# Optimization experiments

Hardware: AMD Instinct MI355X
Metric: run time of the kernel (lower is better)

Reference implementation:

```python
import jax, jax.numpy as jnp
import numpy as np

N = 100000
E = 1600000
IN, HID, OUT = 64, 128, 64
EPS = 1e-5


def _sage_conv(x, src, dst, w_l, b_l, w_r):
    # PyG SAGEConv (mean aggr): out = lin_l(mean_{j in N(i)} x_j) + lin_r(x_i)
    msgs = x[src]                                   # [E, d] gather
    agg = jax.ops.segment_sum(msgs, dst, num_segments=N)  # [N, d]
    deg = jax.ops.segment_sum(jnp.ones((E,), x.dtype), dst, num_segments=N)
    agg = agg / jnp.maximum(deg, 1.0)[:, None]      # mean over neighbors
    return agg @ w_l.T + b_l + x @ w_r.T


def _bn_eval(x, gamma, beta, mean, var):
    return (x - mean) * jax.lax.rsqrt(var + EPS) * gamma + beta


def setup_inputs() -> dict:
    key = jax.random.key(0)
    ks = jax.random.split(key, 16)
    x = jax.random.normal(ks[0], (N, IN), jnp.float32)
    edge_index = jax.random.randint(ks[1], (2, E), 0, N, jnp.int32)
    s1 = 1.0 / np.sqrt(IN)
    s2 = 1.0 / np.sqrt(HID)
    return {
        "x": x,
        "edge_index": edge_index,
        "w1l": jax.random.uniform(ks[2], (HID, IN), jnp.float32, -s1, s1),
        "b1l": jax.random.uniform(ks[3], (HID,), jnp.float32, -s1, s1),
        "w1r": jax.random.uniform(ks[4], (HID, IN), jnp.float32, -s1, s1),
        "bn1_gamma": jax.random.uniform(ks[5], (HID,), jnp.float32, 0.5, 1.5),
        "bn1_beta": jax.random.normal(ks[6], (HID,), jnp.float32) * 0.1,
        "bn1_mean": jax.random.normal(ks[7], (HID,), jnp.float32) * 0.1,
        "bn1_var": jax.random.uniform(ks[8], (HID,), jnp.float32, 0.5, 1.5),
        "w2l": jax.random.uniform(ks[9], (OUT, HID), jnp.float32, -s2, s2),
        "b2l": jax.random.uniform(ks[10], (OUT,), jnp.float32, -s2, s2),
        "w2r": jax.random.uniform(ks[11], (OUT, HID), jnp.float32, -s2, s2),
        "bn2_gamma": jax.random.uniform(ks[12], (OUT,), jnp.float32, 0.5, 1.5),
        "bn2_beta": jax.random.normal(ks[13], (OUT,), jnp.float32) * 0.1,
        "bn2_mean": jax.random.normal(ks[14], (OUT,), jnp.float32) * 0.1,
        "bn2_var": jax.random.uniform(ks[15], (OUT,), jnp.float32, 0.5, 1.5),
    }


def reference(x, edge_index, w1l, b1l, w1r, bn1_gamma, bn1_beta, bn1_mean, bn1_var,
              w2l, b2l, w2r, bn2_gamma, bn2_beta, bn2_mean, bn2_var):
    src, dst = edge_index[0], edge_index[1]
    # layer 1: SAGEConv -> BN -> ReLU (dropout is identity in eval mode)
    h = _sage_conv(x, src, dst, w1l, b1l, w1r)
    h = jax.nn.relu(_bn_eval(h, bn1_gamma, bn1_beta, bn1_mean, bn1_var))
    # layer 2: SAGEConv -> BN
    h = _sage_conv(h, src, dst, w2l, b2l, w2r)
    return _bn_eval(h, bn2_gamma, bn2_beta, bn2_mean, bn2_var)
```

## Files before the change

### kernel.cpp

```cpp
#include <hip/hip_runtime.h>

#define NN 100000
#define NE 1600000
#define EPSV 1e-5f

#define NBUK 196
#define TILE 2048
#define NTIL 782
#define NPREP 6250
#define CAP  9216

typedef __attribute__((ext_vector_type(8))) short bf16x8;
typedef __attribute__((ext_vector_type(4))) float f32x4;

__device__ inline unsigned short f2bf(float f) {
  unsigned u = __builtin_bit_cast(unsigned, f);
  unsigned r = u + 0x7FFFu + ((u >> 16) & 1u);
  return (unsigned short)(r >> 16);
}
__device__ inline float bf2f(unsigned short s) {
  unsigned u = ((unsigned)s) << 16;
  return __builtin_bit_cast(float, u);
}

__device__ __forceinline__ void gload_lds16(const unsigned short* g, unsigned short* l) {
  __builtin_amdgcn_global_load_lds(
      (const __attribute__((address_space(1))) void*)g,
      (__attribute__((address_space(3))) void*)l, 16, 0, 0);
}

__global__ __launch_bounds__(256) void k_binprep(const int* __restrict__ src,
                                                 const int* __restrict__ dst,
                                                 unsigned* __restrict__ pairs,
                                                 int* __restrict__ tileCnt,
                                                 int* __restrict__ tileLo,
                                                 const float* __restrict__ x,
                                                 unsigned short* __restrict__ xb,
                                                 const float* __restrict__ w1l,
                                                 const float* __restrict__ w1r,
                                                 const float* __restrict__ w2l,
                                                 const float* __restrict__ w2r,
                                                 const float* __restrict__ b1l,
                                                 const float* __restrict__ g1,
                                                 const float* __restrict__ be1,
                                                 const float* __restrict__ m1,
                                                 const float* __restrict__ v1,
                                                 const float* __restrict__ b2l,
                                                 const float* __restrict__ g2,
                                                 const float* __restrict__ be2,
                                                 const float* __restrict__ m2,
                                                 const float* __restrict__ v2,
                                                 unsigned short* __restrict__ w1c,
                                                 unsigned short* __restrict__ w2c,
                                                 float* __restrict__ bn) {
  const int tid = threadIdx.x;
  if (blockIdx.x >= NTIL) {
    const int pb = blockIdx.x - NTIL;
    const int gi = pb * 256 + tid;
    float4 v = *(const float4*)(x + (size_t)gi * 4);
    ushort4 o;
    o.x = f2bf(v.x); o.y = f2bf(v.y); o.z = f2bf(v.z); o.w = f2bf(v.w);
    *(ushort4*)(xb + (size_t)gi * 4) = o;
    if (pb < 64) {
      int i = pb * 256 + tid;
      int oo = i >> 7, k = i & 127;
      float vv1 = (k < 64) ? w1l[oo * 64 + k] : w1r[oo * 64 + (k - 64)];
      w1c[i] = f2bf(vv1);
      float vv2 = (oo < 64) ? w2l[oo * 128 + k] : w2r[(oo - 64) * 128 + k];
      w2c[i] = f2bf(vv2);
      if (i < 128) {
        float sc = g1[i] * rsqrtf(v1[i] + EPSV);
        bn[i] = sc;
        bn[128 + i] = (b1l[i] - m1[i]) * sc + be1[i];
      }
      if (i < 64) {
        float sc = g2[i] * rsqrtf(v2[i] + EPSV);
        bn[256 + i] = sc;
        bn[320 + i] = (b2l[i] - m2[i]) * sc + be2[i];
      }
    }
    return;
  }
  __shared__ int cnt[NBUK];
  __shared__ int lo[NBUK];
  __shared__ int ts[256];
  __shared__ unsigned stage[TILE];
  const int t = blockIdx.x;
  const int e0 = t * TILE;
  const int m = min(TILE, NE - e0);

  int dreg[8], sreg[8];
#pragma unroll
  for (int u = 0; u < 8; ++u) {
    int i = u * 256 + tid;
    if (i < m) {
      dreg[u] = dst[e0 + i];
      sreg[u] = src[e0 + i];
    } else {
      dreg[u] = -1;
    }
  }

  for (int i = tid; i < NBUK; i += 256) cnt[i] = 0;
  __syncthreads();
#pragma unroll
  for (int u = 0; u < 8; ++u) {
    if (dreg[u] >= 0) atomicAdd(&cnt[dreg[u] >> 9], 1);
  }
  __syncthreads();
  int c = (tid < NBUK) ? cnt[tid] : 0;
  ts[tid] = c;
  __syncthreads();
  for (int d = 1; d < 256; d <<= 1) {
    int v = (tid >= d) ? ts[tid - d] : 0;
    __syncthreads();
    ts[tid] += v;
    __syncthreads();
  }
  if (tid < NBUK) {
    int ex = ts[tid] - c;
    lo[tid] = ex;
    cnt[tid] = ex;
  }
  __syncthreads();
#pragma unroll
  for (int u = 0; u < 8; ++u) {
    if (dreg[u] >= 0) {
      int pos = atomicAdd(&cnt[dreg[u] >> 9], 1);
      stage[pos] = ((unsigned)(dreg[u] & 511) << 17) | (unsigned)sreg[u];
    }
  }
  __syncthreads();
  for (int i = tid; i < m; i += 256) pairs[(size_t)t * TILE + i] = stage[i];
  if (tid < NBUK) {
    tileCnt[t * NBUK + tid] = cnt[tid] - lo[tid];
    tileLo[t * NBUK + tid] = lo[tid];
  }
}

__global__ __launch_bounds__(256) void k_colscan(const int* __restrict__ tileCnt,
                                                 int* __restrict__ colBase) {
  __shared__ int ts[256];
  const int tid = threadIdx.x;
  const int b = blockIdx.x;
  int v[4];
  int s = 0;
#pragma unroll
  for (int j = 0; j < 4; ++j) {
    int tt = tid * 4 + j;
    v[j] = (tt < NTIL) ? tileCnt[tt * NBUK + b] : 0;
    s += v[j];
  }
  ts[tid] = s;
  __syncthreads();
  for (int d = 1; d < 256; d <<= 1) {
    int x = (tid >= d) ? ts[tid - d] : 0;
    __syncthreads();
    ts[tid] += x;
    __syncthreads();
  }
  int run = ts[tid] - s;
#pragma unroll
  for (int j = 0; j < 4; ++j) {
    int tt = tid * 4 + j;
    if (tt < NTIL) colBase[(size_t)b * NTIL + tt] = run;
    run += v[j];
  }
}

__global__ __launch_bounds__(512) void k_build(const unsigned* __restrict__ pairs,
                                               const int* __restrict__ tileCnt,
                                               const int* __restrict__ tileLo,
                                               const int* __restrict__ colBase,
                                               int* __restrict__ deg,
                                               int* __restrict__ offset,
                                               int* __restrict__ csr) {
  __shared__ unsigned stageA[CAP];
  __shared__ unsigned stageB[CAP];
  __shared__ int colB[NTIL];
  __shared__ int tLo[NTIL];
  __shared__ int hist[512];
  __shared__ int ts[512];
  __shared__ int obase_sh, count_sh;
  const int tid = threadIdx.x;
  const int b = blockIdx.x;
  const int nbase = b * 512;
  const int nloc = min(512, NN - nbase);

  int tb = 0;
  if (tid < NBUK) {
    int cb = colBase[(size_t)tid * NTIL + (NTIL - 1)];
    int tc = tileCnt[(NTIL - 1) * NBUK + tid];
    tb = min(cb + tc, CAP);
  }
  ts[tid] = tb;
  __syncthreads();
  for (int d = 1; d < 512; d <<= 1) {
    int v = (tid >= d) ? ts[tid - d] : 0;
    __syncthreads();
    ts[tid] += v;
    __syncthreads();
  }
  if (tid == b) { obase_sh = ts[tid] - tb; count_sh = tb; }
  for (int i = tid; i < NTIL; i += 512) {
    colB[i] = colBase[(size_t)b * NTIL + i];
    tLo[i] = tileLo[i * NBUK + b];
  }
  hist[tid] = 0;
  __syncthreads();
  const int obase = obase_sh;
  const int count = count_sh;

  for (int i = tid; i < count; i += 512) {
    int a = 0, z = NTIL - 1;
    while (a < z) {
      int mid = (a + z + 1) >> 1;
      if (colB[mid] <= i) a = mid; else z = mid - 1;
    }
    stageA[i] = pairs[(size_t)a * TILE + tLo[a] + (i - colB[a])];
  }
  __syncthreads();
  for (int i = tid; i < count; i += 512) {
    atomicAdd(&hist[stageA[i] >> 17], 1);
  }
  __syncthreads();
  int s = hist[tid];
  ts[tid] = s;
  __syncthreads();
  for (int d = 1; d < 512; d <<= 1) {
    int v = (tid >= d) ? ts[tid - d] : 0;
    __syncthreads();
    ts[tid] += v;
    __syncthreads();
  }
  int ex = ts[tid] - s;
  if (tid < nloc) {
    deg[nbase + tid] = s;
    offset[nbase + tid] = obase + ex;
  }
  hist[tid] = ex;
  __syncthreads();
  for (int i = tid; i < count; i += 512) {
    unsigned e = stageA[i];
    int pos = atomicAdd(&hist[e >> 17], 1);
    stageB[pos] = e & 0x1FFFFu;
  }
  __syncthreads();
  for (int i = tid; i < count; i += 512) csr[obase + i] = (int)stageB[i];
}

__global__ __launch_bounds__(256) void k_aggregate(const unsigned short* __restrict__ xb,
                                                   const int* __restrict__ deg,
                                                   const int* __restrict__ offset,
                                                   const int* __restrict__ csr,
                                                   unsigned short* __restrict__ aggB) {
  int tid = threadIdx.x;
  int node = blockIdx.x * 32 + (tid >> 3);
  int j = tid & 7;
  int cnt = deg[node];
  const int* arow = csr + offset[node];
  float a0=0.f,a1=0.f,a2=0.f,a3=0.f,a4=0.f,a5=0.f,a6=0.f,a7=0.f;
  int k = 0;
  for (; k + 8 <= cnt; k += 8) {
    int s[8];
#pragma unroll
    for (int u = 0; u < 8; ++u) s[u] = arow[k + u];
    uint4 v[8];
#pragma unroll
    for (int u = 0; u < 8; ++u) v[u] = *(const uint4*)(xb + (size_t)s[u] * 64 + j * 8);
#pragma unroll
    for (int u = 0; u < 8; ++u) {
      a0 += bf2f(v[u].x & 0xffff); a1 += bf2f(v[u].x >> 16);
      a2 += bf2f(v[u].y & 0xffff); a3 += bf2f(v[u].y >> 16);
      a4 += bf2f(v[u].z & 0xffff); a5 += bf2f(v[u].z >> 16);
      a6 += bf2f(v[u].w & 0xffff); a7 += bf2f(v[u].w >> 16);
    }
  }
  if (k + 4 <= cnt) {
    int s[4];
#pragma unroll
    for (int u = 0; u < 4; ++u) s[u] = arow[k + u];
    uint4 v[4];
#pragma unroll
    for (int u = 0; u < 4; ++u) v[u] = *(const uint4*)(xb + (size_t)s[u] * 64 + j * 8);
#pragma unroll
    for (int u = 0; u < 4; ++u) {
      a0 += bf2f(v[u].x & 0xffff); a1 += bf2f(v[u].x >> 16);
      a2 += bf2f(v[u].y & 0xffff); a3 += bf2f(v[u].y >> 16);
      a4 += bf2f(v[u].z & 0xffff); a5 += bf2f(v[u].z >> 16);
      a6 += bf2f(v[u].w & 0xffff); a7 += bf2f(v[u].w >> 16);
    }
    k += 4;
  }
  for (; k < cnt; ++k) {
    int s = arow[k];
    uint4 v = *(const uint4*)(xb + (size_t)s * 64 + j * 8);
    a0 += bf2f(v.x & 0xffff); a1 += bf2f(v.x >> 16);
    a2 += bf2f(v.y & 0xffff); a3 += bf2f(v.y >> 16);
    a4 += bf2f(v.z & 0xffff); a5 += bf2f(v.z >> 16);
    a6 += bf2f(v.w & 0xffff); a7 += bf2f(v.w >> 16);
  }
  float inv = 1.0f / fmaxf((float)cnt, 1.0f);
  ushort4 r0, r1;
  r0.x = f2bf(a0 * inv); r0.y = f2bf(a1 * inv); r0.z = f2bf(a2 * inv); r0.w = f2bf(a3 * inv);
  r1.x = f2bf(a4 * inv); r1.y = f2bf(a5 * inv); r1.z = f2bf(a6 * inv); r1.w = f2bf(a7 * inv);
  *(ushort4*)(aggB + (size_t)node * 64 + j * 8) = r0;
  *(ushort4*)(aggB + (size_t)node * 64 + j * 8 + 4) = r1;
}

__global__ __launch_bounds__(512, 1) void k_gemm12(const unsigned short* __restrict__ aggB,
                                                   const unsigned short* __restrict__ xb,
                                                   const unsigned short* __restrict__ w1c,
                                                   const unsigned short* __restrict__ w2c,
                                                   const float* __restrict__ bn,
                                                   unsigned short* __restrict__ t,
                                                   unsigned short* __restrict__ r2) {
  __shared__ unsigned short w1lds[32 * 512];
  __shared__ unsigned short w2lds[32 * 512];
  __shared__ unsigned short hlds[8][2][16 * 128];
  __shared__ float bnlds[384];
  const int tid = threadIdx.x;
  const int w = tid >> 6;
  const int lane = tid & 63;
  const int lr = lane & 15;
  const int q = lane >> 4;
  const int tile = blockIdx.x * 8 + w;
  const int base = tile * 32;
  const int nA = base + lr, nB = base + 16 + lr;
  const int cA = min(nA, NN - 1), cB = min(nB, NN - 1);
  const int swz = (lr & 7) << 4;

#pragma unroll
  for (int it = 0; it < 4; ++it) {
    int idx = it * 512 + tid;
    int f = idx >> 6, l = idx & 63;
    int gofs = ((f >> 2) * 16 + (l & 15)) * 128 + (f & 3) * 32 + (l >> 4) * 8;
    gload_lds16(w1c + gofs, &w1lds[(it * 512 + w * 64) * 8]);
    gload_lds16(w2c + gofs, &w2lds[(it * 512 + w * 64) * 8]);
  }
  if (tid < 384) bnlds[tid] = bn[tid];

  bf16x8 fA[4], fB[4];
  {
    const unsigned short* a = aggB + (size_t)cA * 64 + q * 8;
    const unsigned short* xx = xb + (size_t)cA * 64 + q * 8;
    fA[0] = *(const bf16x8*)a;        fA[1] = *(const bf16x8*)(a + 32);
    fA[2] = *(const bf16x8*)xx;       fA[3] = *(const bf16x8*)(xx + 32);
  }
  {
    const unsigned short* a = aggB + (size_t)cB * 64 + q * 8;
    const unsigned short* xx = xb + (size_t)cB * 64 + q * 8;
    fB[0] = *(const bf16x8*)a;        fB[1] = *(const bf16x8*)(a + 32);
    fB[2] = *(const bf16x8*)xx;       fB[3] = *(const bf16x8*)(xx + 32);
  }
  __syncthreads();
  if (base >= NN) return;

  char* ldsA = (char*)&hlds[w][0][0];
  char* ldsB = (char*)&hlds[w][1][0];

#pragma unroll
  for (int ot = 0; ot < 8; ++ot) {
    const unsigned short* wp = &w1lds[(ot * 4) * 512 + lane * 8];
    bf16x8 w0 = *(const bf16x8*)(wp);
    bf16x8 w1 = *(const bf16x8*)(wp + 512);
    bf16x8 w2 = *(const bf16x8*)(wp + 1024);
    bf16x8 w3 = *(const bf16x8*)(wp + 1536);
    f32x4 aA = {0.f, 0.f, 0.f, 0.f}, aB = {0.f, 0.f, 0.f, 0.f};
    aA = __builtin_amdgcn_mfma_f32_16x16x32_bf16(w0, fA[0], aA, 0, 0, 0);
    aA = __builtin_amdgcn_mfma_f32_16x16x32_bf16(w1, fA[1], aA, 0, 0, 0);
    aA = __builtin_amdgcn_mfma_f32_16x16x32_bf16(w2, fA[2], aA, 0, 0, 0);
    aA = __builtin_amdgcn_mfma_f32_16x16x32_bf16(w3, fA[3], aA, 0, 0, 0);
    aB = __builtin_amdgcn_mfma_f32_16x16x32_bf16(w0, fB[0], aB, 0, 0, 0);
    aB = __builtin_amdgcn_mfma_f32_16x16x32_bf16(w1, fB[1], aB, 0, 0, 0);
    aB = __builtin_amdgcn_mfma_f32_16x16x32_bf16(w2, fB[2], aB, 0, 0, 0);
    aB = __builtin_amdgcn_mfma_f32_16x16x32_bf16(w3, fB[3], aB, 0, 0, 0);
    const int o = ot * 16 + q * 4;
    float4 sc = *(const float4*)&bnlds[o];
    float4 sh = *(const float4*)&bnlds[128 + o];
    ushort4 hA, hB;
    hA.x = f2bf(fmaxf(aA[0] * sc.x + sh.x, 0.f));
    hA.y = f2bf(fmaxf(aA[1] * sc.y + sh.y, 0.f));
    hA.z = f2bf(fmaxf(aA[2] * sc.z + sh.z, 0.f));
    hA.w = f2bf(fmaxf(aA[3] * sc.w + sh.w, 0.f));
    hB.x = f2bf(fmaxf(aB[0] * sc.x + sh.x, 0.f));
    hB.y = f2bf(fmaxf(aB[1] * sc.y + sh.y, 0.f));
    hB.z = f2bf(fmaxf(aB[2] * sc.z + sh.z, 0.f));
    hB.w = f2bf(fmaxf(aB[3] * sc.w + sh.w, 0.f));
    const int wb = lr * 256 + ot * 32 + q * 8;
    *(ushort4*)(ldsA + (wb ^ swz)) = hA;
    *(ushort4*)(ldsB + (wb ^ swz)) = hB;
  }

  bf16x8 hA[4], hB[4];
#pragma unroll
  for (int jj = 0; jj < 4; ++jj) {
    const int rb = lr * 256 + jj * 64 + q * 16;
    hA[jj] = *(const bf16x8*)(ldsA + (rb ^ swz));
    hB[jj] = *(const bf16x8*)(ldsB + (rb ^ swz));
  }

#pragma unroll
  for (int ot = 0; ot < 8; ++ot) {
    const unsigned short* wp = &w2lds[(ot * 4) * 512 + lane * 8];
    bf16x8 w0 = *(const bf16x8*)(wp);
    bf16x8 w1 = *(const bf16x8*)(wp + 512);
    bf16x8 w2 = *(const bf16x8*)(wp + 1024);
    bf16x8 w3 = *(const bf16x8*)(wp + 1536);
    f32x4 aA = {0.f, 0.f, 0.f, 0.f}, aB = {0.f, 0.f, 0.f, 0.f};
    aA = __builtin_amdgcn_mfma_f32_16x16x32_bf16(w0, hA[0], aA, 0, 0, 0);
    aA = __builtin_amdgcn_mfma_f32_16x16x32_bf16(w1, hA[1], aA, 0, 0, 0);
    aA = __builtin_amdgcn_mfma_f32_16x16x32_bf16(w2, hA[2], aA, 0, 0, 0);
    aA = __builtin_amdgcn_mfma_f32_16x16x32_bf16(w3, hA[3], aA, 0, 0, 0);
    aB = __builtin_amdgcn_mfma_f32_16x16x32_bf16(w0, hB[0], aB, 0, 0, 0);
    aB = __builtin_amdgcn_mfma_f32_16x16x32_bf16(w1, hB[1], aB, 0, 0, 0);
    aB = __builtin_amdgcn_mfma_f32_16x16x32_bf16(w2, hB[2], aB, 0, 0, 0);
    aB = __builtin_amdgcn_mfma_f32_16x16x32_bf16(w3, hB[3], aB, 0, 0, 0);
    ushort4 tv;
    if (ot < 4) {
      const int o = ot * 16 + q * 4;
      tv.x = f2bf(aA[0]); tv.y = f2bf(aA[1]); tv.z = f2bf(aA[2]); tv.w = f2bf(aA[3]);
      if (nA < NN) *(ushort4*)(t + (size_t)nA * 64 + o) = tv;
      tv.x = f2bf(aB[0]); tv.y = f2bf(aB[1]); tv.z = f2bf(aB[2]); tv.w = f2bf(aB[3]);
      if (nB < NN) *(ushort4*)(t + (size_t)nB * 64 + o) = tv;
    } else {
      const int o = (ot - 4) * 16 + q * 4;
      tv.x = f2bf(aA[0]); tv.y = f2bf(aA[1]); tv.z = f2bf(aA[2]); tv.w = f2bf(aA[3]);
      if (nA < NN) *(ushort4*)(r2 + (size_t)nA * 64 + o) = tv;
      tv.x = f2bf(aB[0]); tv.y = f2bf(aB[1]); tv.z = f2bf(aB[2]); tv.w = f2bf(aB[3]);
      if (nB < NN) *(ushort4*)(r2 + (size_t)nB * 64 + o) = tv;
    }
  }
}

__global__ __launch_bounds__(256) void k_agg2fin(const unsigned short* __restrict__ t,
                                                 const int* __restrict__ deg,
                                                 const int* __restrict__ offset,
                                                 const int* __restrict__ csr,
                                                 const unsigned short* __restrict__ r2,
                                                 const float* __restrict__ bn,
                                                 float* __restrict__ outp) {
  int tid = threadIdx.x;
  int node = blockIdx.x * 32 + (tid >> 3);
  int j = tid & 7;
  int cnt = deg[node];
  const int* arow = csr + offset[node];
  float a0=0.f,a1=0.f,a2=0.f,a3=0.f,a4=0.f,a5=0.f,a6=0.f,a7=0.f;
  int k = 0;
  for (; k + 8 <= cnt; k += 8) {
    int s[8];
#pragma unroll
    for (int u = 0; u < 8; ++u) s[u] = arow[k + u];
    uint4 v[8];
#pragma unroll
    for (int u = 0; u < 8; ++u) v[u] = *(const uint4*)(t + (size_t)s[u] * 64 + j * 8);
#pragma unroll
    for (int u = 0; u < 8; ++u) {
      a0 += bf2f(v[u].x & 0xffff); a1 += bf2f(v[u].x >> 16);
      a2 += bf2f(v[u].y & 0xffff); a3 += bf2f(v[u].y >> 16);
      a4 += bf2f(v[u].z & 0xffff); a5 += bf2f(v[u].z >> 16);
      a6 += bf2f(v[u].w & 0xffff); a7 += bf2f(v[u].w >> 16);
    }
  }
  if (k + 4 <= cnt) {
    int s[4];
#pragma unroll
    for (int u = 0; u < 4; ++u) s[u] = arow[k + u];
    uint4 v[4];
#pragma unroll
    for (int u = 0; u < 4; ++u) v[u] = *(const uint4*)(t + (size_t)s[u] * 64 + j * 8);
#pragma unroll
    for (int u = 0; u < 4; ++u) {
      a0 += bf2f(v[u].x & 0xffff); a1 += bf2f(v[u].x >> 16);
      a2 += bf2f(v[u].y & 0xffff); a3 += bf2f(v[u].y >> 16);
      a4 += bf2f(v[u].z & 0xffff); a5 += bf2f(v[u].z >> 16);
      a6 += bf2f(v[u].w & 0xffff); a7 += bf2f(v[u].w >> 16);
    }
    k += 4;
  }
  for (; k < cnt; ++k) {
    int s = arow[k];
    uint4 v = *(const uint4*)(t + (size_t)s * 64 + j * 8);
    a0 += bf2f(v.x & 0xffff); a1 += bf2f(v.x >> 16);
    a2 += bf2f(v.y & 0xffff); a3 += bf2f(v.y >> 16);
    a4 += bf2f(v.z & 0xffff); a5 += bf2f(v.z >> 16);
    a6 += bf2f(v.w & 0xffff); a7 += bf2f(v.w >> 16);
  }
  float inv = 1.0f / fmaxf((float)cnt, 1.0f);
  int o = j * 8;
  uint4 rv = *(const uint4*)(r2 + (size_t)node * 64 + o);
  float r0 = bf2f(rv.x & 0xffff), r1 = bf2f(rv.x >> 16);
  float r2a = bf2f(rv.y & 0xffff), r3 = bf2f(rv.y >> 16);
  float r4 = bf2f(rv.z & 0xffff), r5 = bf2f(rv.z >> 16);
  float r6 = bf2f(rv.w & 0xffff), r7 = bf2f(rv.w >> 16);
  float4 sca = *(const float4*)(bn + 256 + o);
  float4 scb = *(const float4*)(bn + 256 + o + 4);
  float4 sha = *(const float4*)(bn + 320 + o);
  float4 shb = *(const float4*)(bn + 320 + o + 4);
  float4 o0, o1;
  o0.x = (a0 * inv + r0) * sca.x + sha.x;
  o0.y = (a1 * inv + r1) * sca.y + sha.y;
  o0.z = (a2 * inv + r2a) * sca.z + sha.z;
  o0.w = (a3 * inv + r3) * sca.w + sha.w;
  o1.x = (a4 * inv + r4) * scb.x + shb.x;
  o1.y = (a5 * inv + r5) * scb.y + shb.y;
  o1.z = (a6 * inv + r6) * scb.z + shb.z;
  o1.w = (a7 * inv + r7) * scb.w + shb.w;
  *(float4*)(outp + (size_t)node * 64 + o) = o0;
  *(float4*)(outp + (size_t)node * 64 + o + 4) = o1;
}

extern "C" void kernel_launch(void* const* d_in, const int* in_sizes, int n_in,
                              void* d_out, int out_size, void* d_ws, size_t ws_size,
                              hipStream_t stream) {
  const float* x   = (const float*)d_in[0];
  const int*   ei  = (const int*)d_in[1];
  const float* w1l = (const float*)d_in[2];
  const float* b1l = (const float*)d_in[3];
  const float* w1r = (const float*)d_in[4];
  const float* g1  = (const float*)d_in[5];
  const float* be1 = (const float*)d_in[6];
  const float* m1  = (const float*)d_in[7];
  const float* v1  = (const float*)d_in[8];
  const float* w2l = (const float*)d_in[9];
  const float* b2l = (const float*)d_in[10];
  const float* w2r = (const float*)d_in[11];
  const float* g2  = (const float*)d_in[12];
  const float* be2 = (const float*)d_in[13];
  const float* m2  = (const float*)d_in[14];
  const float* v2  = (const float*)d_in[15];
  float* outp = (float*)d_out;

  char* ws = (char*)d_ws;
  int*            tileCnt = (int*)ws;
  int*            tileLo  = (int*)(ws + 613120);
  int*            colBase = (int*)(ws + 1226240);
  int*            deg     = (int*)(ws + 1839360);
  int*            offset  = (int*)(ws + 2239360);
  unsigned*       pairs   = (unsigned*)(ws + 2639360);
  int*            csr     = (int*)(ws + 9045504);
  unsigned short* w1c     = (unsigned short*)(ws + 15445504);
  unsigned short* w2c     = (unsigned short*)(ws + 15478272);
  float*          bn      = (float*)(ws + 15511040);
  unsigned short* xb      = (unsigned short*)(ws + 15513088);
  unsigned short* aggB    = (unsigned short*)(ws + 28313088);
  unsigned short* t       = (unsigned short*)(ws + 41113088);
  unsigned short* r2      = (unsigned short*)(ws + 53913088);

  const int* srcp = ei;
  const int* dstp = ei + NE;

  hipLaunchKernelGGL(k_binprep, dim3(NTIL + NPREP), dim3(256), 0, stream,
                     srcp, dstp, pairs, tileCnt, tileLo,
                     x, xb, w1l, w1r, w2l, w2r, b1l, g1, be1, m1, v1,
                     b2l, g2, be2, m2, v2, w1c, w2c, bn);
  hipLaunchKernelGGL(k_colscan, dim3(NBUK), dim3(256), 0, stream,
                     tileCnt, colBase);
  hipLaunchKernelGGL(k_build, dim3(NBUK), dim3(512), 0, stream,
                     pairs, tileCnt, tileLo, colBase, deg, offset, csr);
  hipLaunchKernelGGL(k_aggregate, dim3(NN / 32), dim3(256), 0, stream,
                     xb, deg, offset, csr, aggB);
  hipLaunchKernelGGL(k_gemm12, dim3((NN / 32 + 7) / 8), dim3(512), 0, stream,
                     aggB, xb, w1c, w2c, bn, t, r2);
  hipLaunchKernelGGL(k_agg2fin, dim3(NN / 32), dim3(256), 0, stream,
                     t, deg, offset, csr, r2, bn, outp);
}
```

Baseline: 128.8 us.

## Sort nodes by degree into a permutation for balanced aggregation warps

The CSR build kernel now also records a per-block histogram of node degrees, and a new kernel turns those histograms into a degree-sorted node permutation. Both aggregation kernels walk nodes through this permutation, so each wavefront processes nodes of similar degree and stalls less on its longest-degree lane. The cost is an extra kernel launch, an extra indirection per node, and a loss of spatial locality in the output writes and the per-node reads.

Measured after the change: 255.6 us. +98.5%, slower.

```diff
diff --git a/kernel.cpp b/kernel.cpp
--- a/kernel.cpp
+++ b/kernel.cpp
@@ -174,13 +174,15 @@
                                                const int* __restrict__ colBase,
                                                int* __restrict__ deg,
                                                int* __restrict__ offset,
-                                               int* __restrict__ csr) {
+                                               int* __restrict__ csr,
+                                               int* __restrict__ bdh) {
   __shared__ unsigned stageA[CAP];
   __shared__ unsigned stageB[CAP];
   __shared__ int colB[NTIL];
   __shared__ int tLo[NTIL];
   __shared__ int hist[512];
   __shared__ int ts[512];
+  __shared__ int dh[64];
   __shared__ int obase_sh, count_sh;
   const int tid = threadIdx.x;
   const int b = blockIdx.x;
@@ -194,6 +196,7 @@
     tb = min(cb + tc, CAP);
   }
   ts[tid] = tb;
+  if (tid < 64) dh[tid] = 0;
   __syncthreads();
   for (int d = 1; d < 512; d <<= 1) {
     int v = (tid >= d) ? ts[tid - d] : 0;
@@ -237,9 +240,11 @@
   if (tid < nloc) {
     deg[nbase + tid] = s;
     offset[nbase + tid] = obase + ex;
+    atomicAdd(&dh[min(s, 63)], 1);
   }
   hist[tid] = ex;
   __syncthreads();
+  if (tid < 64) bdh[b * 64 + tid] = dh[tid];
   for (int i = tid; i < count; i += 512) {
     unsigned e = stageA[i];
     int pos = atomicAdd(&hist[e >> 17], 1);
@@ -249,13 +254,44 @@
   for (int i = tid; i < count; i += 512) csr[obase + i] = (int)stageB[i];
 }
 
+__global__ __launch_bounds__(512) void k_perm(const int* __restrict__ bdh,
+                                              const int* __restrict__ deg,
+                                              int* __restrict__ perm) {
+  __shared__ int h[NBUK * 64];
+  __shared__ int cur[64];
+  const int tid = threadIdx.x;
+  const int b = blockIdx.x;
+  for (int i = tid; i < NBUK * 64; i += 512) h[i] = bdh[i];
+  __syncthreads();
+  if (tid < 64) {
+    int binBase = 0;
+    for (int d = 0; d < 64; ++d) {
+      if (d == tid) break;
+      int tot = 0;
+      for (int bb = 0; bb < NBUK; ++bb) tot += h[bb * 64 + d];
+      binBase += tot;
+    }
+    int ro = 0;
+    for (int bb = 0; bb < b; ++bb) ro += h[bb * 64 + tid];
+    cur[tid] = binBase + ro;
+  }
+  __syncthreads();
+  const int node = b * 512 + tid;
+  if (node < NN) {
+    int bin = min(deg[node], 63);
+    int pos = atomicAdd(&cur[bin], 1);
+    perm[pos] = node;
+  }
+}
+
 __global__ __launch_bounds__(256) void k_aggregate(const unsigned short* __restrict__ xb,
                                                    const int* __restrict__ deg,
                                                    const int* __restrict__ offset,
                                                    const int* __restrict__ csr,
+                                                   const int* __restrict__ perm,
                                                    unsigned short* __restrict__ aggB) {
   int tid = threadIdx.x;
-  int node = blockIdx.x * 32 + (tid >> 3);
+  int node = perm[blockIdx.x * 32 + (tid >> 3)];
   int j = tid & 7;
   int cnt = deg[node];
   const int* arow = csr + offset[node];
@@ -437,11 +473,12 @@
                                                  const int* __restrict__ deg,
                                                  const int* __restrict__ offset,
                                                  const int* __restrict__ csr,
+                                                 const int* __restrict__ perm,
                                                  const unsigned short* __restrict__ r2,
                                                  const float* __restrict__ bn,
                                                  float* __restrict__ outp) {
   int tid = threadIdx.x;
-  int node = blockIdx.x * 32 + (tid >> 3);
+  int node = perm[blockIdx.x * 32 + (tid >> 3)];
   int j = tid & 7;
   int cnt = deg[node];
   const int* arow = csr + offset[node];
@@ -542,10 +579,12 @@
   unsigned short* w1c     = (unsigned short*)(ws + 15445504);
   unsigned short* w2c     = (unsigned short*)(ws + 15478272);
   float*          bn      = (float*)(ws + 15511040);
-  unsigned short* xb      = (unsigned short*)(ws + 15513088);
-  unsigned short* aggB    = (unsigned short*)(ws + 28313088);
-  unsigned short* t       = (unsigned short*)(ws + 41113088);
-  unsigned short* r2      = (unsigned short*)(ws + 53913088);
+  int*            bdh     = (int*)(ws + 15513088);
+  int*            perm    = (int*)(ws + 15563264);
+  unsigned short* xb      = (unsigned short*)(ws + 15963264);
+  unsigned short* aggB    = (unsigned short*)(ws + 28763264);
+  unsigned short* t       = (unsigned short*)(ws + 41563264);
+  unsigned short* r2      = (unsigned short*)(ws + 54363264);
 
   const int* srcp = ei;
   const int* dstp = ei + NE;
@@ -557,11 +596,12 @@
   hipLaunchKernelGGL(k_colscan, dim3(NBUK), dim3(256), 0, stream,
                      tileCnt, colBase);
   hipLaunchKernelGGL(k_build, dim3(NBUK), dim3(512), 0, stream,
-                     pairs, tileCnt, tileLo, colBase, deg, offset, csr);
+                     pairs, tileCnt, tileLo, colBase, deg, offset, csr, bdh);
+  hipLaunchKernelGGL(k_perm, dim3(NBUK), dim3(512), 0, stream, bdh, deg, perm);
   hipLaunchKernelGGL(k_aggregate, dim3(NN / 32), dim3(256), 0, stream,
-                     xb, deg, offset, csr, aggB);
+                     xb, deg, offset, csr, perm, aggB);
   hipLaunchKernelGGL(k_gemm12, dim3((NN / 32 + 7) / 8), dim3(512), 0, stream,
                      aggB, xb, w1c, w2c, bn, t, r2);
   hipLaunchKernelGGL(k_agg2fin, dim3(NN / 32), dim3(256), 0, stream,
-                     t, deg, offset, csr, r2, bn, outp);
-}
+                     t, deg, offset, csr, perm, r2, bn, outp);
+}
```
